# Kernel optimization log

Measured on AMD Instinct MI355X. Metric: run time of the kernel, lower is better.

The kernel has to match this reference:

```python
import jax, jax.numpy as jnp
import numpy as np

ALPHA = 0.2  # LeakyReLU negative slope

def setup_inputs() -> dict:
    key = jax.random.key(0)
    k1, k2, k3 = jax.random.split(key, 3)
    B, N, IN_DIM = 16, 1024, 128
    HEADS, HEAD_DIM = 2, 64  # out_dim = 128
    h = jax.random.normal(k1, (B, N, IN_DIM), dtype=jnp.float32)
    # xavier_uniform with gain=1.414 ~ uniform(-b, b); exact init unimportant for correctness
    bW = 1.414 * np.sqrt(6.0 / (IN_DIM + HEAD_DIM))
    W = jax.random.uniform(k2, (HEADS, IN_DIM, HEAD_DIM), minval=-bW, maxval=bW, dtype=jnp.float32)
    ba = 1.414 * np.sqrt(6.0 / (2 * HEAD_DIM + 1))
    a = jax.random.uniform(k3, (HEADS, 2 * HEAD_DIM, 1), minval=-ba, maxval=ba, dtype=jnp.float32)
    return {"h": h, "W": W, "a": a}

def reference(h, W, a):
    B, N, in_dim = h.shape
    heads, _, head_dim = W.shape
    out_dim = heads * head_dim
    # h_prime: [B, N, H, D]
    hp = jnp.einsum('bni,hio->bnho', h, W)
    # Split additive attention: a . [h_i ; h_j] = a_src . h_i + a_dst . h_j (same math as concat)
    a_src = a[:, :head_dim, 0]   # [H, D]
    a_dst = a[:, head_dim:, 0]   # [H, D]
    e_src = jnp.einsum('bnhd,hd->bhn', hp, a_src)  # [B, H, N]
    e_dst = jnp.einsum('bmhd,hd->bhm', hp, a_dst)  # [B, H, N]
    e = e_src[:, :, :, None] + e_dst[:, :, None, :]  # [B, H, N, N]
    e = jnp.where(e >= 0, e, ALPHA * e)  # LeakyReLU(0.2)
    att = jax.nn.softmax(e, axis=-1)
    # dropout p=0.0 (eval-deterministic): no-op
    h_new = jnp.einsum('bhnm,bmho->bnho', att, hp).reshape(B, N, out_dim)
    out = h_new + h if in_dim == out_dim else h_new
    return jax.nn.elu(out)
```

## Files before the change

### kernel.cpp

```cpp
#include <hip/hip_runtime.h>
#include <math.h>


#define LOG2E 1.44269504088896340736f

typedef __bf16 bf16x8 __attribute__((ext_vector_type(8)));
typedef float floatx4 __attribute__((ext_vector_type(4)));

union U16x8 { uint4 u; bf16x8 b; };

__device__ __forceinline__ unsigned short f2bf(float f) {
    union { __bf16 b; unsigned short u; } x;
    x.b = (__bf16)f;
    return x.u;
}

__global__ __launch_bounds__(256) void gat_hp(
    const float* __restrict__ hg,
    const float* __restrict__ Wg,
    const float* __restrict__ ag,
    unsigned short* __restrict__ hpB,
    float* __restrict__ es_g,
    float* __restrict__ ed_g)
{
    const int t = threadIdx.x;
    const int lane = t & 63;
    const int wv = blockIdx.x * 4 + (t >> 6);
    const int rt = wv >> 1;
    const int half = wv & 1;
    const int n0 = rt * 16;
    const int col = lane & 15, quad = lane >> 4;

    floatx4 acc[4];
#pragma unroll
    for (int ct = 0; ct < 4; ++ct) acc[ct] = (floatx4){0.f, 0.f, 0.f, 0.f};

    const float* hrow = hg + (size_t)(n0 + col) * 128;
    const float* wh = Wg + half * 8192;
#pragma unroll
    for (int kq = 0; kq < 4; ++kq) {
        float4 h0 = *(const float4*)(hrow + kq * 32 + quad * 8);
        float4 h1 = *(const float4*)(hrow + kq * 32 + quad * 8 + 4);
        bf16x8 af;
        af[0] = (__bf16)h0.x; af[1] = (__bf16)h0.y;
        af[2] = (__bf16)h0.z; af[3] = (__bf16)h0.w;
        af[4] = (__bf16)h1.x; af[5] = (__bf16)h1.y;
        af[6] = (__bf16)h1.z; af[7] = (__bf16)h1.w;
        const int k0 = kq * 32 + quad * 8;
#pragma unroll
        for (int ct = 0; ct < 4; ++ct) {
            const float* wp = wh + (size_t)k0 * 64 + ct * 16 + col;
            bf16x8 bfr;
#pragma unroll
            for (int j = 0; j < 8; ++j) bfr[j] = (__bf16)wp[j * 64];
            acc[ct] = __builtin_amdgcn_mfma_f32_16x16x32_bf16(af, bfr, acc[ct], 0, 0, 0);
        }
    }

    const int b = n0 >> 10;
    const int nloc = n0 & 1023;
    const int bh = b * 2 + half;

    float esr[4] = {0.f, 0.f, 0.f, 0.f}, edr[4] = {0.f, 0.f, 0.f, 0.f};
#pragma unroll
    for (int ct = 0; ct < 4; ++ct) {
        int d = ct * 16 + col;
        float as = ag[half * 128 + d];
        float ad = ag[half * 128 + 64 + d];
#pragma unroll
        for (int r = 0; r < 4; ++r) {
            esr[r] = fmaf(acc[ct][r], as, esr[r]);
            edr[r] = fmaf(acc[ct][r], ad, edr[r]);
        }
    }
#pragma unroll
    for (int off = 1; off <= 8; off <<= 1) {
#pragma unroll
        for (int r = 0; r < 4; ++r) {
            esr[r] += __shfl_xor(esr[r], off, 64);
            edr[r] += __shfl_xor(edr[r], off, 64);
        }
    }
    if (col == 0) {
        size_t base = (size_t)bh * 1024 + nloc + quad * 4;
#pragma unroll
        for (int r = 0; r < 4; ++r) {
            es_g[base + r] = esr[r];
            ed_g[base + r] = edr[r];
        }
    }

    const int gloc = (nloc >> 3) + (quad >> 1);
#pragma unroll
    for (int ct = 0; ct < 4; ++ct) {
        int d = ct * 16 + col;
        uint2 pk;
        pk.x = (unsigned)f2bf(acc[ct][0]) | ((unsigned)f2bf(acc[ct][1]) << 16);
        pk.y = (unsigned)f2bf(acc[ct][2]) | ((unsigned)f2bf(acc[ct][3]) << 16);
        size_t idx = ((size_t)(bh * 128 + gloc) * 64 + d) * 8 + (quad & 1) * 4;
        *(uint2*)(hpB + idx) = pk;
    }
}

__global__ __launch_bounds__(256, 3) void gat_att(
    const float* __restrict__ hg,
    const unsigned short* __restrict__ hpB,
    const float* __restrict__ es_g,
    const float* __restrict__ ed_g,
    float* __restrict__ out)
{
    __shared__ float red[4 * 64 * 35];

    const int t = threadIdx.x;
    const int lane = t & 63;
    const int w = t >> 6;
    const int bh = blockIdx.x & 31;
    const int nt = blockIdx.x >> 5;
    const int b = bh >> 1, hh = bh & 1;
    const int n0 = nt * 32;
    const int col = lane & 15, quad = lane >> 4;

    const float* edrow = ed_g + (size_t)bh * 1024;

    float mx = -1e30f;
#pragma unroll
    for (int i = 0; i < 4; ++i) {
        float4 v = *(const float4*)(edrow + lane * 16 + i * 4);
        mx = fmaxf(mx, fmaxf(fmaxf(v.x, v.y), fmaxf(v.z, v.w)));
    }
#pragma unroll
    for (int off = 1; off < 64; off <<= 1) mx = fmaxf(mx, __shfl_xor(mx, off, 64));
    const float mxl = mx * LOG2E;

    const float s2a = es_g[(size_t)bh * 1024 + n0 + col] * LOG2E;
    const float s2b = es_g[(size_t)bh * 1024 + n0 + 16 + col] * LOG2E;
    const float x0a = s2a + mxl, x0b = s2b + mxl;
    const float Ma = fmaxf(x0a, 0.2f * x0a), Mb = fmaxf(x0b, 0.2f * x0b);
    const float s2ma = s2a - Ma, s5ma = 0.2f * s2a - Ma;
    const float s2mb = s2b - Mb, s5mb = 0.2f * s2b - Mb;
    const float K = LOG2E, K5 = 0.2f * LOG2E;

    floatx4 acc0[4], acc1[4];
#pragma unroll
    for (int ct = 0; ct < 4; ++ct) {
        acc0[ct] = (floatx4){0.f, 0.f, 0.f, 0.f};
        acc1[ct] = (floatx4){0.f, 0.f, 0.f, 0.f};
    }
    float ls0 = 0.f, ls1 = 0.f;

    const uint4* hb = (const uint4*)hpB + (size_t)bh * 8192;
    const int mbase = w * 256;

    float4 d0 = *(const float4*)(edrow + mbase + quad * 8);
    float4 d1 = *(const float4*)(edrow + mbase + quad * 8 + 4);
    int gm = (mbase >> 3) + quad;
    uint4 bu0 = hb[gm * 64 + col];
    uint4 bu1 = hb[gm * 64 + 16 + col];
    uint4 bu2 = hb[gm * 64 + 32 + col];
    uint4 bu3 = hb[gm * 64 + 48 + col];

#pragma unroll
    for (int i = 0; i < 8; ++i) {
        float4 c0 = d0, c1 = d1;
        uint4 cb0 = bu0, cb1 = bu1, cb2 = bu2, cb3 = bu3;
        if (i < 7) {
            int m1 = mbase + (i + 1) * 32;
            d0 = *(const float4*)(edrow + m1 + quad * 8);
            d1 = *(const float4*)(edrow + m1 + quad * 8 + 4);
            gm = (m1 >> 3) + quad;
            bu0 = hb[gm * 64 + col];
            bu1 = hb[gm * 64 + 16 + col];
            bu2 = hb[gm * 64 + 32 + col];
            bu3 = hb[gm * 64 + 48 + col];
        }
        float dv[8] = {c0.x, c0.y, c0.z, c0.w, c1.x, c1.y, c1.z, c1.w};
        bf16x8 af0, af1;
#pragma unroll
        for (int j = 0; j < 8; ++j) {
            float pa = __builtin_amdgcn_exp2f(fmaxf(fmaf(dv[j], K, s2ma), fmaf(dv[j], K5, s5ma)));
            float pb = __builtin_amdgcn_exp2f(fmaxf(fmaf(dv[j], K, s2mb), fmaf(dv[j], K5, s5mb)));
            ls0 += pa; ls1 += pb;
            af0[j] = (__bf16)pa;
            af1[j] = (__bf16)pb;
        }
        U16x8 u0; u0.u = cb0;
        U16x8 u1; u1.u = cb1;
        U16x8 u2; u2.u = cb2;
        U16x8 u3; u3.u = cb3;
        acc0[0] = __builtin_amdgcn_mfma_f32_16x16x32_bf16(af0, u0.b, acc0[0], 0, 0, 0);
        acc1[0] = __builtin_amdgcn_mfma_f32_16x16x32_bf16(af1, u0.b, acc1[0], 0, 0, 0);
        acc0[1] = __builtin_amdgcn_mfma_f32_16x16x32_bf16(af0, u1.b, acc0[1], 0, 0, 0);
        acc1[1] = __builtin_amdgcn_mfma_f32_16x16x32_bf16(af1, u1.b, acc1[1], 0, 0, 0);
        acc0[2] = __builtin_amdgcn_mfma_f32_16x16x32_bf16(af0, u2.b, acc0[2], 0, 0, 0);
        acc1[2] = __builtin_amdgcn_mfma_f32_16x16x32_bf16(af1, u2.b, acc1[2], 0, 0, 0);
        acc0[3] = __builtin_amdgcn_mfma_f32_16x16x32_bf16(af0, u3.b, acc0[3], 0, 0, 0);
        acc1[3] = __builtin_amdgcn_mfma_f32_16x16x32_bf16(af1, u3.b, acc1[3], 0, 0, 0);
    }

    ls0 += __shfl_xor(ls0, 16, 64); ls0 += __shfl_xor(ls0, 32, 64);
    ls1 += __shfl_xor(ls1, 16, 64); ls1 += __shfl_xor(ls1, 32, 64);

    float* myred = red + (w * 64 + lane) * 35;
#pragma unroll
    for (int ct = 0; ct < 4; ++ct)
#pragma unroll
        for (int r = 0; r < 4; ++r) {
            myred[ct * 4 + r]      = acc0[ct][r];
            myred[16 + ct * 4 + r] = acc1[ct][r];
        }
    myred[32] = ls0;
    myred[33] = ls1;
    __syncthreads();

    const int tile = w & 1;
    const int ctp = w >> 1;
    float ltot = 0.f;
#pragma unroll
    for (int v4 = 0; v4 < 4; ++v4)
        ltot += red[(v4 * 64 + lane) * 35 + 32 + tile];
    float inv[4];
#pragma unroll
    for (int r = 0; r < 4; ++r)
        inv[r] = __builtin_amdgcn_rcpf(__shfl(ltot, quad * 4 + r, 16));

#pragma unroll
    for (int cti = 0; cti < 2; ++cti) {
        const int ct = ctp * 2 + cti;
        float facc[4] = {0.f, 0.f, 0.f, 0.f};
#pragma unroll
        for (int v4 = 0; v4 < 4; ++v4) {
            const float* rr = red + (v4 * 64 + lane) * 35 + tile * 16 + ct * 4;
#pragma unroll
            for (int r = 0; r < 4; ++r) facc[r] += rr[r];
        }
#pragma unroll
        for (int r = 0; r < 4; ++r) {
            int n = n0 + tile * 16 + quad * 4 + r;
            size_t off = (size_t)(b * 1024 + n) * 128 + hh * 64 + ct * 16 + col;
            float vv = facc[r] * inv[r] + hg[off];
            out[off] = vv > 0.f ? vv : __builtin_amdgcn_exp2f(vv * LOG2E) - 1.f;
        }
    }
}

extern "C" void kernel_launch(void* const* d_in, const int* in_sizes, int n_in,
                              void* d_out, int out_size, void* d_ws, size_t ws_size,
                              hipStream_t stream) {
    const float* h = (const float*)d_in[0];
    const float* W = (const float*)d_in[1];
    const float* a = (const float*)d_in[2];
    float* out = (float*)d_out;

    unsigned short* hpB = (unsigned short*)d_ws;
    float* es  = (float*)((char*)d_ws + (4u << 20));
    float* ed  = es + 32 * 1024;

    gat_hp<<<512, 256, 0, stream>>>(h, W, a, hpB, es, ed);
    gat_att<<<1024, 256, 0, stream>>>(h, hpB, es, ed, out);
}
```

Measured before the change: 86.00 us.

## Factor LeakyReLU-softmax exponent into per-node exponentials and prepack W

```diff
diff --git a/kernel.cpp b/kernel.cpp
--- a/kernel.cpp
+++ b/kernel.cpp
@@ -15,13 +15,36 @@
     return x.u;
 }
 
+__global__ __launch_bounds__(256) void gat_prep(
+    const float* __restrict__ Wg,
+    const float* __restrict__ ag,
+    unsigned short* __restrict__ Wp,
+    float* __restrict__ acat)
+{
+    const int t = threadIdx.x;
+    const int base = blockIdx.x * 1024;
+#pragma unroll
+    for (int i = 0; i < 4; ++i) {
+        int idx = base + i * 256 + t;
+        int c = idx & 127, k = idx >> 7;
+        float v = Wg[(c >> 6) * 8192 + k * 64 + (c & 63)];
+        Wp[((k >> 3) * 128 + c) * 8 + (k & 7)] = f2bf(v);
+    }
+    if (blockIdx.x == 0 && t < 128) {
+        acat[t]       = ag[(t >> 6) * 128 + (t & 63)];
+        acat[128 + t] = ag[(t >> 6) * 128 + 64 + (t & 63)];
+    }
+}
+
 __global__ __launch_bounds__(256) void gat_hp(
     const float* __restrict__ hg,
-    const float* __restrict__ Wg,
-    const float* __restrict__ ag,
+    const unsigned short* __restrict__ Wp,
+    const float* __restrict__ acat,
     unsigned short* __restrict__ hpB,
     float* __restrict__ es_g,
-    float* __restrict__ ed_g)
+    float* __restrict__ ed_g,
+    float* __restrict__ e1_g,
+    float* __restrict__ e5_g)
 {
     const int t = threadIdx.x;
     const int lane = t & 63;
@@ -36,7 +59,7 @@
     for (int ct = 0; ct < 4; ++ct) acc[ct] = (floatx4){0.f, 0.f, 0.f, 0.f};
 
     const float* hrow = hg + (size_t)(n0 + col) * 128;
-    const float* wh = Wg + half * 8192;
+    const uint4* wp4 = (const uint4*)Wp;
 #pragma unroll
     for (int kq = 0; kq < 4; ++kq) {
         float4 h0 = *(const float4*)(hrow + kq * 32 + quad * 8);
@@ -46,14 +69,11 @@
         af[2] = (__bf16)h0.z; af[3] = (__bf16)h0.w;
         af[4] = (__bf16)h1.x; af[5] = (__bf16)h1.y;
         af[6] = (__bf16)h1.z; af[7] = (__bf16)h1.w;
-        const int k0 = kq * 32 + quad * 8;
+        const uint4* wbase = wp4 + (size_t)(kq * 4 + quad) * 128 + half * 64;
 #pragma unroll
         for (int ct = 0; ct < 4; ++ct) {
-            const float* wp = wh + (size_t)k0 * 64 + ct * 16 + col;
-            bf16x8 bfr;
-#pragma unroll
-            for (int j = 0; j < 8; ++j) bfr[j] = (__bf16)wp[j * 64];
-            acc[ct] = __builtin_amdgcn_mfma_f32_16x16x32_bf16(af, bfr, acc[ct], 0, 0, 0);
+            U16x8 bu; bu.u = wbase[ct * 16 + col];
+            acc[ct] = __builtin_amdgcn_mfma_f32_16x16x32_bf16(af, bu.b, acc[ct], 0, 0, 0);
         }
     }
 
@@ -64,9 +84,8 @@
     float esr[4] = {0.f, 0.f, 0.f, 0.f}, edr[4] = {0.f, 0.f, 0.f, 0.f};
 #pragma unroll
     for (int ct = 0; ct < 4; ++ct) {
-        int d = ct * 16 + col;
-        float as = ag[half * 128 + d];
-        float ad = ag[half * 128 + 64 + d];
+        int c = half * 64 + ct * 16 + col;
+        float as = acat[c], ad = acat[128 + c];
 #pragma unroll
         for (int r = 0; r < 4; ++r) {
             esr[r] = fmaf(acc[ct][r], as, esr[r]);
@@ -87,6 +106,8 @@
         for (int r = 0; r < 4; ++r) {
             es_g[base + r] = esr[r];
             ed_g[base + r] = edr[r];
+            e1_g[base + r] = __builtin_amdgcn_exp2f(edr[r] * LOG2E);
+            e5_g[base + r] = __builtin_amdgcn_exp2f(edr[r] * (0.2f * LOG2E));
         }
     }
 
@@ -102,11 +123,13 @@
     }
 }
 
-__global__ __launch_bounds__(256, 3) void gat_att(
+__global__ __launch_bounds__(256, 2) void gat_att(
     const float* __restrict__ hg,
     const unsigned short* __restrict__ hpB,
     const float* __restrict__ es_g,
     const float* __restrict__ ed_g,
+    const float* __restrict__ e1_g,
+    const float* __restrict__ e5_g,
     float* __restrict__ out)
 {
     __shared__ float red[4 * 64 * 35];
@@ -121,6 +144,8 @@
     const int col = lane & 15, quad = lane >> 4;
 
     const float* edrow = ed_g + (size_t)bh * 1024;
+    const float* e1row = e1_g + (size_t)bh * 1024;
+    const float* e5row = e5_g + (size_t)bh * 1024;
 
     float mx = -1e30f;
 #pragma unroll
@@ -136,9 +161,10 @@
     const float s2b = es_g[(size_t)bh * 1024 + n0 + 16 + col] * LOG2E;
     const float x0a = s2a + mxl, x0b = s2b + mxl;
     const float Ma = fmaxf(x0a, 0.2f * x0a), Mb = fmaxf(x0b, 0.2f * x0b);
-    const float s2ma = s2a - Ma, s5ma = 0.2f * s2a - Ma;
-    const float s2mb = s2b - Mb, s5mb = 0.2f * s2b - Mb;
-    const float K = LOG2E, K5 = 0.2f * LOG2E;
+    const float C2a = __builtin_amdgcn_exp2f(s2a - Ma);
+    const float C5a = __builtin_amdgcn_exp2f(0.2f * s2a - Ma);
+    const float C2b = __builtin_amdgcn_exp2f(s2b - Mb);
+    const float C5b = __builtin_amdgcn_exp2f(0.2f * s2b - Mb);
 
     floatx4 acc0[4], acc1[4];
 #pragma unroll
@@ -151,8 +177,10 @@
     const uint4* hb = (const uint4*)hpB + (size_t)bh * 8192;
     const int mbase = w * 256;
 
-    float4 d0 = *(const float4*)(edrow + mbase + quad * 8);
-    float4 d1 = *(const float4*)(edrow + mbase + quad * 8 + 4);
+    float4 d0 = *(const float4*)(e1row + mbase + quad * 8);
+    float4 d1 = *(const float4*)(e1row + mbase + quad * 8 + 4);
+    float4 f0 = *(const float4*)(e5row + mbase + quad * 8);
+    float4 f1 = *(const float4*)(e5row + mbase + quad * 8 + 4);
     int gm = (mbase >> 3) + quad;
     uint4 bu0 = hb[gm * 64 + col];
     uint4 bu1 = hb[gm * 64 + 16 + col];
@@ -161,24 +189,27 @@
 
 #pragma unroll
     for (int i = 0; i < 8; ++i) {
-        float4 c0 = d0, c1 = d1;
+        float4 c0 = d0, c1 = d1, g0 = f0, g1 = f1;
         uint4 cb0 = bu0, cb1 = bu1, cb2 = bu2, cb3 = bu3;
         if (i < 7) {
             int m1 = mbase + (i + 1) * 32;
-            d0 = *(const float4*)(edrow + m1 + quad * 8);
-            d1 = *(const float4*)(edrow + m1 + quad * 8 + 4);
+            d0 = *(const float4*)(e1row + m1 + quad * 8);
+            d1 = *(const float4*)(e1row + m1 + quad * 8 + 4);
+            f0 = *(const float4*)(e5row + m1 + quad * 8);
+            f1 = *(const float4*)(e5row + m1 + quad * 8 + 4);
             gm = (m1 >> 3) + quad;
             bu0 = hb[gm * 64 + col];
             bu1 = hb[gm * 64 + 16 + col];
             bu2 = hb[gm * 64 + 32 + col];
             bu3 = hb[gm * 64 + 48 + col];
         }
-        float dv[8] = {c0.x, c0.y, c0.z, c0.w, c1.x, c1.y, c1.z, c1.w};
+        float ev[8] = {c0.x, c0.y, c0.z, c0.w, c1.x, c1.y, c1.z, c1.w};
+        float fv[8] = {g0.x, g0.y, g0.z, g0.w, g1.x, g1.y, g1.z, g1.w};
         bf16x8 af0, af1;
 #pragma unroll
         for (int j = 0; j < 8; ++j) {
-            float pa = __builtin_amdgcn_exp2f(fmaxf(fmaf(dv[j], K, s2ma), fmaf(dv[j], K5, s5ma)));
-            float pb = __builtin_amdgcn_exp2f(fmaxf(fmaf(dv[j], K, s2mb), fmaf(dv[j], K5, s5mb)));
+            float pa = fmaxf(ev[j] * C2a, fv[j] * C5a);
+            float pb = fmaxf(ev[j] * C2b, fv[j] * C5b);
             ls0 += pa; ls1 += pb;
             af0[j] = (__bf16)pa;
             af1[j] = (__bf16)pb;
@@ -254,7 +285,12 @@
     unsigned short* hpB = (unsigned short*)d_ws;
     float* es  = (float*)((char*)d_ws + (4u << 20));
     float* ed  = es + 32 * 1024;
-
-    gat_hp<<<512, 256, 0, stream>>>(h, W, a, hpB, es, ed);
-    gat_att<<<1024, 256, 0, stream>>>(h, hpB, es, ed, out);
-}
+    float* e1  = ed + 32 * 1024;
+    float* e5  = e1 + 32 * 1024;
+    unsigned short* Wp = (unsigned short*)(e5 + 32 * 1024);
+    float* acat = (float*)((char*)Wp + 16384 * sizeof(unsigned short));
+
+    gat_prep<<<16, 256, 0, stream>>>(W, a, Wp, acat);
+    gat_hp<<<512, 256, 0, stream>>>(h, Wp, acat, hpB, es, ed, e1, e5);
+    gat_att<<<1024, 256, 0, stream>>>(h, hpB, es, ed, e1, e5, out);
+}
```

Result: no change. 84.35 us (-1.9%).
